# Kernel tuning notes

Hardware: AMD Instinct MI355X
Metric: run time of the kernel (lower is better)

## Reference

```python
import jax, jax.numpy as jnp
import numpy as np

N_NODES = 50000
IN_CH = 128
OUT_CH = 64
N_EDGES = 800000
K_HOPS = 2


def setup_inputs() -> dict:
    key = jax.random.key(0)
    k1, k2, k3, k4 = jax.random.split(key, 4)
    x = jax.random.normal(k1, (N_NODES, IN_CH), dtype=jnp.float32)
    edge_index = jax.random.randint(k2, (2, N_EDGES), 0, N_NODES, dtype=jnp.int64)
    # SGC linear layer params (torch Linear default init approx)
    scale = 1.0 / np.sqrt(IN_CH)
    W = jax.random.uniform(k3, (IN_CH, OUT_CH), dtype=jnp.float32, minval=-scale, maxval=scale)
    b = jax.random.uniform(k4, (OUT_CH,), dtype=jnp.float32, minval=-scale, maxval=scale)
    return {"x": x, "edge_index": edge_index, "W": W, "b": b}


def _sgc_propagate(x, row, col, K):
    # GCN symmetric normalization with self-loops: S = D^-1/2 (A+I) D^-1/2
    n = x.shape[0]
    loop = jnp.arange(n, dtype=row.dtype)
    row = jnp.concatenate([row, loop])
    col = jnp.concatenate([col, loop])
    ones = jnp.ones(row.shape[0], dtype=x.dtype)
    deg = jax.ops.segment_sum(ones, col, num_segments=n)
    dinv = jnp.where(deg > 0, jax.lax.rsqrt(deg), 0.0)
    norm = dinv[row] * dinv[col]  # [E+N]
    for _ in range(K):
        # gather source features, weight, scatter-add to targets
        msg = norm[:, None] * x[row]  # [E+N, C]
        x = jax.ops.segment_sum(msg, col, num_segments=n)
    return x


def reference(x, edge_index, W, b):
    # Dropout is identity in eval mode (deterministic reference).
    row, col = edge_index[0], edge_index[1]
    h = _sgc_propagate(x, row, col, K_HOPS)  # [N, IN_CH]
    return h @ W + b  # [N, OUT_CH]
```

## Files before the change

### kernel.cpp

```cpp
#include <hip/hip_runtime.h>

#define N_NODES 50000
#define IN_CH   128
#define OUT_CH  64
#define N_EDGES 800000
#define NBINS   49
#define LBCAP   128
#define BINCAP  20000
#define PCAP    64
#define WT_STR  136
#define SA_B    500
#define SA_E    1600
#define SB_B    49
#define GEMM_BL 196


using short8  = __attribute__((ext_vector_type(8))) short;
using float4v = __attribute__((ext_vector_type(4))) float;

__device__ __forceinline__ unsigned int bpack(float a, float b) {
    unsigned int ua = __float_as_uint(a), ub = __float_as_uint(b);
    unsigned int ra = (ua + 0x7fffu + ((ua >> 16) & 1u)) >> 16;
    unsigned int rb = (ub + 0x7fffu + ((ub >> 16) & 1u)) & 0xffff0000u;
    return (ra & 0xffffu) | rb;
}

__global__ __launch_bounds__(256) void scatter_a(const int* __restrict__ row,
        const int* __restrict__ col, unsigned int* __restrict__ binbuf,
        int* __restrict__ gcur) {
    __shared__ unsigned int sbuf[NBINS][LBCAP];
    __shared__ int scnt[NBINS];
    __shared__ int sdst[NBINS];
    const int tid = threadIdx.x;
    if (tid < NBINS) scnt[tid] = 0;
    __syncthreads();
    const int e0 = blockIdx.x * SA_E;
    for (int i = tid; i < SA_E / 4; i += 256) {
        int e = e0 + i * 4;
        int4 t4 = *(const int4*)&col[e];
        int4 s4 = *(const int4*)&row[e];
        const int ts[4] = { t4.x, t4.y, t4.z, t4.w };
        const int ss[4] = { s4.x, s4.y, s4.z, s4.w };
        #pragma unroll
        for (int j = 0; j < 4; ++j) {
            int b = ts[j] >> 10;
            int pos = atomicAdd(&scnt[b], 1);
            if (pos < LBCAP)
                sbuf[b][pos] = ((unsigned)(ts[j] & 1023) << 16) | (unsigned)ss[j];
        }
    }
    __syncthreads();
    if (tid < NBINS) {
        int c = scnt[tid]; if (c > LBCAP) c = LBCAP; scnt[tid] = c;
        sdst[tid] = atomicAdd(&gcur[tid], c);
    }
    __syncthreads();
    const int wave = tid >> 6, lane = tid & 63;
    for (int b = wave; b < NBINS; b += 4) {
        int c = scnt[b];
        size_t d = (size_t)b * BINCAP + sdst[b];
        for (int i = lane; i < c; i += 64)
            binbuf[d + i] = sbuf[b][i];
    }
}

__global__ __launch_bounds__(1024) void scatb_gemm(
        const unsigned int* __restrict__ binbuf, const int* __restrict__ gcur,
        unsigned short* __restrict__ esrc, unsigned char* __restrict__ fill8,
        const float* __restrict__ x, const float* __restrict__ W,
        float* __restrict__ y) {
    const int bid = blockIdx.x, tid = threadIdx.x;
    if (bid < SB_B) {
        __shared__ int lcnt[1024];
        const int t0 = bid << 10;
        lcnt[tid] = 0;
        __syncthreads();
        int cnt = gcur[bid]; if (cnt > BINCAP) cnt = BINCAP;
        const unsigned int* src = binbuf + (size_t)bid * BINCAP;
        for (int i = tid; i < cnt; i += 1024) {
            unsigned int e = src[i];
            int tl = e >> 16;
            int pos = atomicAdd(&lcnt[tl], 1);
            int t = t0 + tl;
            if (pos < PCAP && t < N_NODES)
                esrc[(size_t)pos * N_NODES + t] = (unsigned short)(e & 0xffffu);
        }
        __syncthreads();
        int t = t0 + tid;
        if (t < N_NODES) {
            int v = lcnt[tid]; if (v > PCAP) v = PCAP;
            fill8[t] = (unsigned char)v;
        }
        return;
    }
    __shared__ unsigned short sWT[64 * WT_STR];
    for (int i = tid; i < IN_CH * OUT_CH; i += 1024) {
        int k = i >> 6, c = i & 63;
        unsigned int u = __float_as_uint(W[i]);
        u = (u + 0x7fffu + ((u >> 16) & 1u)) >> 16;
        sWT[c * WT_STR + k] = (unsigned short)u;
    }
    __syncthreads();
    const int lane = tid & 63;
    const int quad = lane >> 4;
    const int c15  = lane & 15;
    const int tile = (bid - SB_B) * 16 + (tid >> 6);
    if (tile >= N_NODES / 16) return;

    short8 bf[4][4];
    #pragma unroll
    for (int t = 0; t < 4; ++t)
        #pragma unroll
        for (int ch = 0; ch < 4; ++ch)
            bf[ch][t] = *(const short8*)&sWT[(t * 16 + c15) * WT_STR + ch * 32 + quad * 8];

    const float* xr = x + ((size_t)tile * 16 + c15) * IN_CH;
    float4v acc[4] = {{0.f,0.f,0.f,0.f},{0.f,0.f,0.f,0.f},
                      {0.f,0.f,0.f,0.f},{0.f,0.f,0.f,0.f}};
    #pragma unroll
    for (int ch = 0; ch < 4; ++ch) {
        float4 f0 = *(const float4*)(xr + ch * 32 + quad * 8);
        float4 f1 = *(const float4*)(xr + ch * 32 + quad * 8 + 4);
        unsigned int d0 = bpack(f0.x, f0.y), d1 = bpack(f0.z, f0.w);
        unsigned int d2 = bpack(f1.x, f1.y), d3 = bpack(f1.z, f1.w);
        short8 a8;
        a8[0] = (short)d0; a8[1] = (short)(d0 >> 16);
        a8[2] = (short)d1; a8[3] = (short)(d1 >> 16);
        a8[4] = (short)d2; a8[5] = (short)(d2 >> 16);
        a8[6] = (short)d3; a8[7] = (short)(d3 >> 16);
        #pragma unroll
        for (int t = 0; t < 4; ++t)
            acc[t] = __builtin_amdgcn_mfma_f32_16x16x32_bf16(a8, bf[ch][t], acc[t], 0, 0, 0);
    }
    #pragma unroll
    for (int t = 0; t < 4; ++t)
        #pragma unroll
        for (int r = 0; r < 4; ++r)
            y[((size_t)tile * 16 + quad * 4 + r) * OUT_CH + t * 16 + c15] = acc[t][r];
}

__global__ __launch_bounds__(256) void scale_z0(const float* __restrict__ y,
        const unsigned char* __restrict__ fill8, uint4* __restrict__ z0) {
    int gid = blockIdx.x * 256 + threadIdx.x;
    if (gid >= N_NODES * 8) return;
    int n = gid >> 3, q = gid & 7;
    float d = rsqrtf((float)((int)fill8[n] + 1));
    float4 a = ((const float4*)y)[n * 16 + q * 2];
    float4 b = ((const float4*)y)[n * 16 + q * 2 + 1];
    uint4 pk;
    pk.x = bpack(d * a.x, d * a.y);
    pk.y = bpack(d * a.z, d * a.w);
    pk.z = bpack(d * b.x, d * b.y);
    pk.w = bpack(d * b.z, d * b.w);
    z0[gid] = pk;
}

__global__ __launch_bounds__(256) void hop_gather(const uint4* __restrict__ hin,
        void* __restrict__ hout, const unsigned char* __restrict__ fill8,
        const unsigned short* __restrict__ esrc, const float* __restrict__ bias,
        int last) {
    int lane = threadIdx.x & 63;
    int g = lane >> 3;
    int q = lane & 7;
    int t = __builtin_amdgcn_readfirstlane(blockIdx.x * 4 + (threadIdx.x >> 6));
    if (t >= N_NODES) return;
    int deg = fill8[t];

    float acc[8] = {};
    if (g == 0) {
        uint4 r = hin[t * 8 + q];
        const unsigned int rw[4] = { r.x, r.y, r.z, r.w };
        #pragma unroll
        for (int j = 0; j < 4; ++j) {
            acc[2 * j]     = __uint_as_float(rw[j] << 16);
            acc[2 * j + 1] = __uint_as_float(rw[j] & 0xffff0000u);
        }
    }
    for (int base = 0; base < deg; base += 8) {
        int e = base + g;
        if (e < deg) {
            int s = (int)esrc[(size_t)e * N_NODES + t];
            uint4 r = hin[s * 8 + q];
            const unsigned int rw[4] = { r.x, r.y, r.z, r.w };
            #pragma unroll
            for (int j = 0; j < 4; ++j) {
                acc[2 * j]     += __uint_as_float(rw[j] << 16);
                acc[2 * j + 1] += __uint_as_float(rw[j] & 0xffff0000u);
            }
        }
    }
    #pragma unroll
    for (int j = 0; j < 8; ++j) {
        acc[j] += __shfl_xor(acc[j], 8);
        acc[j] += __shfl_xor(acc[j], 16);
        acc[j] += __shfl_xor(acc[j], 32);
    }
    if (g == 0) {
        if (!last) {
            float rdeg = 1.0f / (float)(deg + 1);
            uint4 pk;
            pk.x = bpack(acc[0] * rdeg, acc[1] * rdeg);
            pk.y = bpack(acc[2] * rdeg, acc[3] * rdeg);
            pk.z = bpack(acc[4] * rdeg, acc[5] * rdeg);
            pk.w = bpack(acc[6] * rdeg, acc[7] * rdeg);
            ((uint4*)hout)[t * 8 + q] = pk;
        } else {
            float d = rsqrtf((float)(deg + 1));
            float4 b0 = ((const float4*)bias)[q * 2];
            float4 b1 = ((const float4*)bias)[q * 2 + 1];
            float4 o0 = make_float4(d * acc[0] + b0.x, d * acc[1] + b0.y,
                                    d * acc[2] + b0.z, d * acc[3] + b0.w);
            float4 o1 = make_float4(d * acc[4] + b1.x, d * acc[5] + b1.y,
                                    d * acc[6] + b1.z, d * acc[7] + b1.w);
            ((float4*)hout)[t * 16 + q * 2]     = o0;
            ((float4*)hout)[t * 16 + q * 2 + 1] = o1;
        }
    }
}

extern "C" void kernel_launch(void* const* d_in, const int* in_sizes, int n_in,
                              void* d_out, int out_size, void* d_ws, size_t ws_size,
                              hipStream_t stream) {
    const float* x  = (const float*)d_in[0];
    const int*   ei = (const int*)d_in[1];
    const float* W  = (const float*)d_in[2];
    const float* b  = (const float*)d_in[3];
    float*       out = (float*)d_out;

    const int* row = ei;
    const int* col = ei + N_EDGES;

    char* ws = (char*)d_ws;
    size_t a = 0;
    auto alloc = [&](size_t bytes) { char* p = ws + a; a = (a + bytes + 255) & ~(size_t)255; return p; };
    int*            gcur   = (int*)           alloc(NBINS * sizeof(int));
    unsigned int*   binbuf = (unsigned int*)  alloc((size_t)NBINS * BINCAP * 4);
    unsigned short* esrc   = (unsigned short*)alloc((size_t)PCAP * N_NODES * 2);
    unsigned char*  fill8  = (unsigned char*) alloc(N_NODES);
    float*          y      = (float*)         alloc((size_t)N_NODES * OUT_CH * 4);
    unsigned int*   z0     = (unsigned int*)  alloc((size_t)N_NODES * OUT_CH * 2);
    unsigned int*   z1     = (unsigned int*)  alloc((size_t)N_NODES * OUT_CH * 2);

    hipMemsetAsync(gcur, 0, NBINS * sizeof(int), stream);

    const int B = 256;
    int gS = (N_NODES * 8 + B - 1) / B;
    int gH = (N_NODES + 3) / 4;

    scatter_a<<<SA_B, B, 0, stream>>>(row, col, binbuf, gcur);
    scatb_gemm<<<SB_B + GEMM_BL, 1024, 0, stream>>>(binbuf, gcur, esrc, fill8, x, W, y);
    scale_z0 <<<gS, B, 0, stream>>>(y, fill8, (uint4*)z0);
    hop_gather<<<gH, B, 0, stream>>>((const uint4*)z0, (void*)z1, fill8, esrc, b, 0);
    hop_gather<<<gH, B, 0, stream>>>((const uint4*)z1, (void*)out, fill8, esrc, b, 1);
}
```

Before: 167.0 us.

## Split hop gather into channel halves with XCD-aware block remap

Stores the bf16 intermediate features as two separate 32-channel planes, and runs the gather kernel as two passes of blocks, one per half. Each plane is about 3.2MB, so it fits better in per-XCD L2 during random gathers. Block indices are remapped so each XCD processes a contiguous range of target nodes. Each lane now covers 4 uint4 chunks with 16 edges in flight, and stores are nontemporal. The cost is that every edge index is read twice, once per half, and one extra shuffle-reduction step is added.

```diff
diff --git a/kernel.cpp b/kernel.cpp
--- a/kernel.cpp
+++ b/kernel.cpp
@@ -13,10 +13,13 @@
 #define SA_E    1600
 #define SB_B    49
 #define GEMM_BL 196
+#define HOP_HB  12500
+#define ZPL     (N_NODES * 4)
 
 
 using short8  = __attribute__((ext_vector_type(8))) short;
 using float4v = __attribute__((ext_vector_type(4))) float;
+using uint4v  = __attribute__((ext_vector_type(4))) unsigned int;
 
 __device__ __forceinline__ unsigned int bpack(float a, float b) {
     unsigned int ua = __float_as_uint(a), ub = __float_as_uint(b);
@@ -140,35 +143,45 @@
 }
 
 __global__ __launch_bounds__(256) void scale_z0(const float* __restrict__ y,
-        const unsigned char* __restrict__ fill8, uint4* __restrict__ z0) {
+        const unsigned char* __restrict__ fill8, uint4v* __restrict__ z0) {
     int gid = blockIdx.x * 256 + threadIdx.x;
     if (gid >= N_NODES * 8) return;
     int n = gid >> 3, q = gid & 7;
+    int half = q >> 2, qq = q & 3;
     float d = rsqrtf((float)((int)fill8[n] + 1));
     float4 a = ((const float4*)y)[n * 16 + q * 2];
     float4 b = ((const float4*)y)[n * 16 + q * 2 + 1];
-    uint4 pk;
+    uint4v pk;
     pk.x = bpack(d * a.x, d * a.y);
     pk.y = bpack(d * a.z, d * a.w);
     pk.z = bpack(d * b.x, d * b.y);
     pk.w = bpack(d * b.z, d * b.w);
-    z0[gid] = pk;
-}
-
-__global__ __launch_bounds__(256) void hop_gather(const uint4* __restrict__ hin,
+    z0[(size_t)half * ZPL + n * 4 + qq] = pk;
+}
+
+__global__ __launch_bounds__(256) void hop_gather(const uint4v* __restrict__ hin,
         void* __restrict__ hout, const unsigned char* __restrict__ fill8,
         const unsigned short* __restrict__ esrc, const float* __restrict__ bias,
         int last) {
+    int b = blockIdx.x;
+    int half = (b >= HOP_HB) ? 1 : 0;
+    int orig = b - half * HOP_HB;
+    int xcd = orig & 7;
+    int idx = orig >> 3;
+    int cbase = (xcd < 4) ? xcd * 1563 : 4 * 1563 + (xcd - 4) * 1562;
+    int wg = cbase + idx;
+
     int lane = threadIdx.x & 63;
-    int g = lane >> 3;
-    int q = lane & 7;
-    int t = __builtin_amdgcn_readfirstlane(blockIdx.x * 4 + (threadIdx.x >> 6));
+    int g = lane >> 2;
+    int q = lane & 3;
+    int t = __builtin_amdgcn_readfirstlane(wg * 4 + (threadIdx.x >> 6));
     if (t >= N_NODES) return;
     int deg = fill8[t];
+    const uint4v* hp = hin + (size_t)half * ZPL;
 
     float acc[8] = {};
     if (g == 0) {
-        uint4 r = hin[t * 8 + q];
+        uint4v r = hp[t * 4 + q];
         const unsigned int rw[4] = { r.x, r.y, r.z, r.w };
         #pragma unroll
         for (int j = 0; j < 4; ++j) {
@@ -176,11 +189,11 @@
             acc[2 * j + 1] = __uint_as_float(rw[j] & 0xffff0000u);
         }
     }
-    for (int base = 0; base < deg; base += 8) {
+    for (int base = 0; base < deg; base += 16) {
         int e = base + g;
         if (e < deg) {
             int s = (int)esrc[(size_t)e * N_NODES + t];
-            uint4 r = hin[s * 8 + q];
+            uint4v r = hp[s * 4 + q];
             const unsigned int rw[4] = { r.x, r.y, r.z, r.w };
             #pragma unroll
             for (int j = 0; j < 4; ++j) {
@@ -191,6 +204,7 @@
     }
     #pragma unroll
     for (int j = 0; j < 8; ++j) {
+        acc[j] += __shfl_xor(acc[j], 4);
         acc[j] += __shfl_xor(acc[j], 8);
         acc[j] += __shfl_xor(acc[j], 16);
         acc[j] += __shfl_xor(acc[j], 32);
@@ -198,22 +212,23 @@
     if (g == 0) {
         if (!last) {
             float rdeg = 1.0f / (float)(deg + 1);
-            uint4 pk;
+            uint4v pk;
             pk.x = bpack(acc[0] * rdeg, acc[1] * rdeg);
             pk.y = bpack(acc[2] * rdeg, acc[3] * rdeg);
             pk.z = bpack(acc[4] * rdeg, acc[5] * rdeg);
             pk.w = bpack(acc[6] * rdeg, acc[7] * rdeg);
-            ((uint4*)hout)[t * 8 + q] = pk;
+            __builtin_nontemporal_store(pk,
+                (uint4v*)hout + (size_t)half * ZPL + t * 4 + q);
         } else {
             float d = rsqrtf((float)(deg + 1));
-            float4 b0 = ((const float4*)bias)[q * 2];
-            float4 b1 = ((const float4*)bias)[q * 2 + 1];
-            float4 o0 = make_float4(d * acc[0] + b0.x, d * acc[1] + b0.y,
-                                    d * acc[2] + b0.z, d * acc[3] + b0.w);
-            float4 o1 = make_float4(d * acc[4] + b1.x, d * acc[5] + b1.y,
-                                    d * acc[6] + b1.z, d * acc[7] + b1.w);
-            ((float4*)hout)[t * 16 + q * 2]     = o0;
-            ((float4*)hout)[t * 16 + q * 2 + 1] = o1;
+            float4 b0 = ((const float4*)bias)[half * 8 + q * 2];
+            float4 b1 = ((const float4*)bias)[half * 8 + q * 2 + 1];
+            float4v o0 = { d * acc[0] + b0.x, d * acc[1] + b0.y,
+                           d * acc[2] + b0.z, d * acc[3] + b0.w };
+            float4v o1 = { d * acc[4] + b1.x, d * acc[5] + b1.y,
+                           d * acc[6] + b1.z, d * acc[7] + b1.w };
+            __builtin_nontemporal_store(o0, (float4v*)hout + t * 16 + half * 8 + q * 2);
+            __builtin_nontemporal_store(o1, (float4v*)hout + t * 16 + half * 8 + q * 2 + 1);
         }
     }
 }
@@ -245,11 +260,11 @@
 
     const int B = 256;
     int gS = (N_NODES * 8 + B - 1) / B;
-    int gH = (N_NODES + 3) / 4;
+    int gH = 2 * HOP_HB;
 
     scatter_a<<<SA_B, B, 0, stream>>>(row, col, binbuf, gcur);
     scatb_gemm<<<SB_B + GEMM_BL, 1024, 0, stream>>>(binbuf, gcur, esrc, fill8, x, W, y);
-    scale_z0 <<<gS, B, 0, stream>>>(y, fill8, (uint4*)z0);
-    hop_gather<<<gH, B, 0, stream>>>((const uint4*)z0, (void*)z1, fill8, esrc, b, 0);
-    hop_gather<<<gH, B, 0, stream>>>((const uint4*)z1, (void*)out, fill8, esrc, b, 1);
-}
+    scale_z0 <<<gS, B, 0, stream>>>(y, fill8, (uint4v*)z0);
+    hop_gather<<<gH, B, 0, stream>>>((const uint4v*)z0, (void*)z1, fill8, esrc, b, 0);
+    hop_gather<<<gH, B, 0, stream>>>((const uint4v*)z1, (void*)out, fill8, esrc, b, 1);
+}
```

New measurement: 192.2 us. +15.1%, slower.
